# Performance work log

Hardware: AMD Instinct MI355X
Metric: run time of the kernel (lower is better)

Reference implementation:

```python
import jax, jax.numpy as jnp
import numpy as np


def conv1d(x, w, b):
    # x: [B, C_in, T], w: [C_out, C_in, K] (torch layout), b: [C_out]
    y = jax.lax.conv_general_dilated(
        x, w, window_strides=(1,), padding='SAME',
        dimension_numbers=('NCH', 'OIH', 'NCH'))
    return y + b[None, :, None]


def setup_inputs() -> dict:
    B, T, IN, H, D, K = 16, 2048, 80, 512, 512, 1024
    key = jax.random.key(0)
    ks = jax.random.split(key, 10)
    f32 = jnp.float32

    def w_init(k, shape, fan_in):
        return (jax.random.normal(k, shape, f32) / np.sqrt(fan_in)).astype(f32)

    return {
        'mels':    jax.random.normal(ks[0], (B, T, IN), f32),
        'enc_w1':  w_init(ks[1], (H, IN, 3), IN * 3),
        'enc_b1':  jnp.zeros((H,), f32),
        'enc_w2':  w_init(ks[2], (D, H, 3), H * 3),
        'enc_b2':  jnp.zeros((D,), f32),
        'codebook': jax.random.normal(ks[3], (K, D), f32),
        'dec_w1':  w_init(ks[4], (H, D, 3), D * 3),
        'dec_b1':  jnp.zeros((H,), f32),
        'dec_w2':  w_init(ks[5], (IN, H, 3), H * 3),
        'dec_b2':  jnp.zeros((IN,), f32),
    }


def reference(mels, enc_w1, enc_b1, enc_w2, enc_b2, codebook,
              dec_w1, dec_b1, dec_w2, dec_b2):
    B, T, _ = mels.shape
    D = codebook.shape[1]

    # ---- encoder: conv -> relu -> conv ----
    x = jnp.swapaxes(mels, 1, 2)                      # [B, in_dim, T]
    z = conv1d(jax.nn.relu(conv1d(x, enc_w1, enc_b1)), enc_w2, enc_b2)  # [B, D, T]

    # ---- vector quantization ----
    z_t = jnp.swapaxes(z, 1, 2)                       # [B, T, D]
    flat = z_t.reshape(-1, D)                         # [B*T, D]
    d = ((flat ** 2).sum(axis=1, keepdims=True)
         - 2.0 * flat @ codebook.T
         + (codebook ** 2).sum(axis=1)[None, :])      # [B*T, K]
    idx = jnp.argmin(d, axis=1).reshape(B, T)         # [B, T] int
    quantized = codebook[idx]                         # [B, T, D] gather

    # ---- decoder: conv -> relu -> conv ----
    q = jnp.swapaxes(quantized, 1, 2)                 # [B, D, T]
    recon = conv1d(jax.nn.relu(conv1d(q, dec_w1, dec_b1)), dec_w2, dec_b2)
    recon = jnp.swapaxes(recon, 1, 2)                 # [B, T, in_dim]
    return recon, idx
```

## Files before the change

### kernel.cpp

```cpp
#include <hip/hip_runtime.h>
#include <hip/hip_bf16.h>

#define Bsz   16
#define Tn    2048
#define INC   80
#define Hc    512
#define Dc    512
#define NCODE 1024
#define BT    (Bsz * Tn)
#define RECON_N (Bsz * Tn * INC)
#define MARGIN 0.03f

typedef __attribute__((ext_vector_type(8))) short bf16x8;
typedef __attribute__((ext_vector_type(4))) float f32x4;
typedef __attribute__((ext_vector_type(4))) unsigned short u16x4;

static __device__ __forceinline__ unsigned short f2bf(float x) {
    unsigned u = __float_as_uint(x);
    u += 0x7FFF + ((u >> 16) & 1);
    return (unsigned short)(u >> 16);
}
static __device__ __forceinline__ float bf2f(unsigned short h) {
    return __uint_as_float((unsigned)h << 16);
}

typedef const __attribute__((address_space(1))) unsigned int* gas_p;
typedef __attribute__((address_space(3))) unsigned int* las_p;
static __device__ __forceinline__ void async16(const void* g, const void* l) {
    __builtin_amdgcn_global_load_lds(
        (gas_p)(unsigned long long)g,
        (las_p)(unsigned int)(unsigned long long)l,
        16, 0, 0);
}

__global__ __launch_bounds__(64)
void code_norms(const float* __restrict__ CB, float* __restrict__ CN) {
    int j = blockIdx.x;
    int lane = threadIdx.x;
    const float4* row = (const float4*)(CB + (size_t)j * Dc);
    float s = 0.f;
    #pragma unroll
    for (int i = 0; i < 2; ++i) {
        float4 v = row[lane + i * 64];
        s = fmaf(v.x, v.x, s);
        s = fmaf(v.y, v.y, s);
        s = fmaf(v.z, v.z, s);
        s = fmaf(v.w, v.w, s);
    }
    #pragma unroll
    for (int off = 32; off > 0; off >>= 1) s += __shfl_down(s, off, 64);
    if (lane == 0) CN[j] = s;
}

__global__ __launch_bounds__(256)
void cb_transpose(const float* __restrict__ CB, float* __restrict__ CBt) {
    const int j0 = blockIdx.x * 64;
    const int d0 = blockIdx.y * 64;
    __shared__ float ts[64][65];
    const int tid = threadIdx.x;
    for (int i = tid; i < 4096; i += 256) {
        int r = i >> 6, c = i & 63;
        ts[r][c] = CB[(size_t)(j0 + r) * Dc + d0 + c];
    }
    __syncthreads();
    for (int i = tid; i < 4096; i += 256) {
        int r = i >> 6, c = i & 63;
        CBt[(size_t)(d0 + r) * NCODE + j0 + c] = ts[c][r];
    }
}

__global__ __launch_bounds__(256)
void mels_transpose(const float* __restrict__ M, float* __restrict__ MT) {
    const int t0 = blockIdx.x * 64;
    const int b  = blockIdx.y;
    __shared__ float ts[64][84];
    const int tid = threadIdx.x;
    #pragma unroll
    for (int it = 0; it < 5; ++it) {
        int i = tid + it * 256;
        int t = i / 20, c4 = i % 20;
        *(float4*)&ts[t][c4 * 4] =
            *(const float4*)&M[((size_t)b * Tn + t0 + t) * INC + c4 * 4];
    }
    __syncthreads();
    #pragma unroll
    for (int it = 0; it < 20; ++it) {
        int i = tid + it * 256;
        int c = i >> 6, t = i & 63;
        MT[((size_t)b * INC + c) * Tn + t0 + t] = ts[t][c];
    }
}

__global__ __launch_bounds__(256)
void wt_transpose(const float* __restrict__ W, float* __restrict__ Wt,
                  int Cin, int Cout) {
    const int o0 = blockIdx.x * 64;
    const int c0 = blockIdx.y * 16;
    __shared__ float ts[48][65];
    const int tid = threadIdx.x;
    for (int i = tid; i < 64 * 48; i += 256) {
        int o = i / 48, ck = i % 48;
        int oo = o0 + o;
        float v = 0.f;
        if (oo < Cout) v = W[(size_t)oo * Cin * 3 + c0 * 3 + ck];
        ts[ck][o] = v;
    }
    __syncthreads();
    for (int i = tid; i < 48 * 64; i += 256) {
        int o = i & 63, ck = i >> 6;
        int oo = o0 + o;
        if (oo < Cout) Wt[(size_t)(c0 * 3 + ck) * Cout + oo] = ts[ck][o];
    }
}

__global__ __launch_bounds__(256)
void wsplit(const float* __restrict__ W, unsigned short* __restrict__ Whi,
            unsigned short* __restrict__ Wlo) {
    int o = blockIdx.x, k = blockIdx.y;
    #pragma unroll
    for (int it = 0; it < 2; ++it) {
        int c = threadIdx.x + it * 256;
        float v = W[((size_t)o * Hc + c) * 3 + k];
        unsigned short h = f2bf(v);
        Whi[((size_t)k * Hc + o) * Hc + c] = h;
        Wlo[((size_t)k * Hc + o) * Hc + c] = f2bf(v - bf2f(h));
    }
}

__global__ __launch_bounds__(256)
void wsplit80(const float* __restrict__ W, unsigned short* __restrict__ Wh) {
    int o = blockIdx.x, k = blockIdx.y;
    #pragma unroll
    for (int it = 0; it < 2; ++it) {
        int c = threadIdx.x + it * 256;
        Wh[((size_t)k * INC + o) * Hc + c] = f2bf(W[((size_t)o * Hc + c) * 3 + k]);
    }
}

__global__ __launch_bounds__(256)
void cbsplit(const float* __restrict__ CB, unsigned short* __restrict__ CBh,
             unsigned short* __restrict__ CBl) {
    int j = blockIdx.x;
    #pragma unroll
    for (int it = 0; it < 2; ++it) {
        int d = threadIdx.x + it * 256;
        float v = CB[(size_t)j * Dc + d];
        unsigned short h = f2bf(v);
        CBh[(size_t)j * Dc + d] = h;
        CBl[(size_t)j * Dc + d] = f2bf(v - bf2f(h));
    }
}

__global__ __launch_bounds__(256)
void conv_enc1(const float* __restrict__ X, const float* __restrict__ Wt,
               const float* __restrict__ bias, float* __restrict__ Y) {
    const int t0 = blockIdx.x * 64;
    const int o0 = blockIdx.y * 128;
    const int b  = blockIdx.z;
    __shared__ __align__(16) float Xs[16][72];
    __shared__ __align__(16) float Ws[48][132];
    const int tid = threadIdx.x;
    const int tx = tid & 15, ty = tid >> 4;
    float acc[8][4] = {};
    const float* Xb = X + (size_t)b * INC * Tn;

    for (int c0 = 0; c0 < INC; c0 += 16) {
        for (int i = tid; i < 16 * 66; i += 256) {
            int cc = i / 66, tt = i % 66;
            int t = t0 + tt - 1;
            float v = 0.f;
            if (t >= 0 && t < Tn) v = Xb[(size_t)(c0 + cc) * Tn + t];
            Xs[cc][tt] = v;
        }
        for (int i = tid; i < 48 * 128; i += 256) {
            int o = i & 127, ck = i >> 7;
            Ws[ck][o] = Wt[(size_t)(c0 * 3 + ck) * Hc + o0 + o];
        }
        __syncthreads();
        #pragma unroll
        for (int cc = 0; cc < 16; ++cc) {
            float4 xa = *(const float4*)&Xs[cc][tx * 4];
            float2 xb2 = *(const float2*)&Xs[cc][tx * 4 + 4];
            float xv[6] = {xa.x, xa.y, xa.z, xa.w, xb2.x, xb2.y};
            #pragma unroll
            for (int k = 0; k < 3; ++k) {
                float4 wa = *(const float4*)&Ws[cc * 3 + k][ty * 4];
                float4 wb = *(const float4*)&Ws[cc * 3 + k][64 + ty * 4];
                float wv[8] = {wa.x, wa.y, wa.z, wa.w, wb.x, wb.y, wb.z, wb.w};
                #pragma unroll
                for (int i8 = 0; i8 < 8; ++i8)
                    #pragma unroll
                    for (int j = 0; j < 4; ++j)
                        acc[i8][j] = fmaf(wv[i8], xv[k + j], acc[i8][j]);
            }
        }
        __syncthreads();
    }
    float* Yb = Y + (size_t)b * Hc * Tn;
    #pragma unroll
    for (int og = 0; og < 2; ++og)
        #pragma unroll
        for (int oi = 0; oi < 4; ++oi) {
            int o = o0 + og * 64 + ty * 4 + oi;
            float bv = bias[o];
            const int i8 = og * 4 + oi;
            float4 r;
            r.x = fmaxf(acc[i8][0] + bv, 0.f);
            r.y = fmaxf(acc[i8][1] + bv, 0.f);
            r.z = fmaxf(acc[i8][2] + bv, 0.f);
            r.w = fmaxf(acc[i8][3] + bv, 0.f);
            *(float4*)&Yb[(size_t)o * Tn + t0 + tx * 4] = r;
        }
}

__global__ __launch_bounds__(256)
void zero_guards(unsigned short* __restrict__ Yhl) {
    const int b = blockIdx.x;
    u16x4 z = {0, 0, 0, 0};
    size_t r0 = (size_t)(b * (Tn + 2)) * 1024;
    size_t r1 = (size_t)(b * (Tn + 2) + Tn + 1) * 1024;
    *(u16x4*)(Yhl + r0 + threadIdx.x * 4) = z;
    *(u16x4*)(Yhl + r1 + threadIdx.x * 4) = z;
}

__global__ __launch_bounds__(256)
void split_t(const float* __restrict__ X, unsigned short* __restrict__ Yhl,
             int rowStride, int rowOff) {
    const int t0 = blockIdx.x * 64;
    const int c0 = blockIdx.y * 64;
    const int b  = blockIdx.z;
    __shared__ __align__(16) float ts[64][68];
    const int tid = threadIdx.x;
    #pragma unroll
    for (int it = 0; it < 4; ++it) {
        int i = tid + it * 256;
        int cc = i >> 4, t4 = i & 15;
        float4 v = *(const float4*)&X[((size_t)b * Hc + c0 + cc) * Tn + t0 + t4 * 4];
        ts[t4 * 4 + 0][cc] = v.x;
        ts[t4 * 4 + 1][cc] = v.y;
        ts[t4 * 4 + 2][cc] = v.z;
        ts[t4 * 4 + 3][cc] = v.w;
    }
    __syncthreads();
    #pragma unroll
    for (int it = 0; it < 4; ++it) {
        int i = tid + it * 256;
        int t = i >> 4, c4 = i & 15;
        int c = c0 + c4 * 4;
        float4 v = *(const float4*)&ts[t][c4 * 4];
        float va[4] = {v.x, v.y, v.z, v.w};
        u16x4 h, l;
        #pragma unroll
        for (int r = 0; r < 4; ++r) {
            unsigned short hh = f2bf(va[r]);
            h[r] = hh;
            l[r] = f2bf(va[r] - bf2f(hh));
        }
        size_t base = ((size_t)(b * rowStride + rowOff + t0 + t) * 16 + (c >> 5)) * 64
                      + (c & 31);
        *(u16x4*)(Yhl + base) = h;
        *(u16x4*)(Yhl + base + 32) = l;
    }
}

__global__ __launch_bounds__(256)
void conv_mid_mfma(const unsigned short* __restrict__ Xhl,
                   const unsigned short* __restrict__ Whi,
                   const unsigned short* __restrict__ Wlo,
                   const float* __restrict__ bias,
                   float* __restrict__ Y) {
    const int t0 = blockIdx.x * 128;
    const int o0 = blockIdx.y * 128;
    const int b  = blockIdx.z;
    __shared__ __align__(16) unsigned short XL[2][136 * 64];
    const int tid  = threadIdx.x;
    const int lane = tid & 63;
    const int wave = tid >> 6;
    const int wm = wave >> 1, wn = wave & 1;
    const int m16 = lane & 15;
    const int q = lane >> 4;
    const int lrow = lane >> 3;
    const int lchk = (lane & 7) ^ lrow;
    const unsigned short* Xb = Xhl + ((size_t)b * (Tn + 2) + t0) * 1024
                               + (size_t)lrow * 1024 + lchk * 8;

    f32x4 acc[4][4];
    #pragma unroll
    for (int mt = 0; mt < 4; ++mt)
        #pragma unroll
        for (int nt = 0; nt < 4; ++nt)
            acc[mt][nt] = (f32x4){0.f, 0.f, 0.f, 0.f};

    #pragma unroll
    for (int i = 0; i < 5; ++i) {
        int ii = wave + i * 4;
        if (ii < 17)
            async16(Xb + (size_t)ii * 8192, &XL[0][ii * 512]);
    }

    for (int c0 = 0; c0 < Hc; c0 += 32) {
        const int buf = (c0 >> 5) & 1;
        __syncthreads();
        if (c0 + 32 < Hc) {
            const unsigned short* src = Xb + (size_t)((c0 >> 5) + 1) * 64;
            #pragma unroll
            for (int i = 0; i < 5; ++i) {
                int ii = wave + i * 4;
                if (ii < 17)
                    async16(src + (size_t)ii * 8192, &XL[buf ^ 1][ii * 512]);
            }
        }
        #pragma unroll
        for (int k = 0; k < 3; ++k) {
            bf16x8 Ah[4], Al[4];
            #pragma unroll
            for (int mt = 0; mt < 4; ++mt) {
                int o = o0 + wm * 64 + mt * 16 + m16;
                size_t base = (size_t)(k * Hc + o) * Hc + c0 + q * 8;
                Ah[mt] = *(const bf16x8*)(Whi + base);
                Al[mt] = *(const bf16x8*)(Wlo + base);
            }
            #pragma unroll
            for (int nt = 0; nt < 4; ++nt) {
                int row = wn * 64 + nt * 16 + m16 + k;
                const unsigned short* rp = &XL[buf][row * 64];
                int ph = (q ^ (row & 7)) * 8;
                union { bf16x8 v; uint4 u; } bh, bl;
                bh.u = *(const uint4*)(rp + ph);
                bl.u = *(const uint4*)(rp + (ph ^ 32));
                #pragma unroll
                for (int mt = 0; mt < 4; ++mt)
                    acc[mt][nt] = __builtin_amdgcn_mfma_f32_16x16x32_bf16(
                        Ah[mt], bh.v, acc[mt][nt], 0, 0, 0);
                #pragma unroll
                for (int mt = 0; mt < 4; ++mt)
                    acc[mt][nt] = __builtin_amdgcn_mfma_f32_16x16x32_bf16(
                        Al[mt], bh.v, acc[mt][nt], 0, 0, 0);
                #pragma unroll
                for (int mt = 0; mt < 4; ++mt)
                    acc[mt][nt] = __builtin_amdgcn_mfma_f32_16x16x32_bf16(
                        Ah[mt], bl.v, acc[mt][nt], 0, 0, 0);
            }
        }
    }
    float* Yb = Y + (size_t)b * Hc * Tn;
    #pragma unroll
    for (int mt = 0; mt < 4; ++mt) {
        int ob = o0 + wm * 64 + mt * 16 + q * 4;
        float4 bq = *(const float4*)&bias[ob];
        float bqa[4] = {bq.x, bq.y, bq.z, bq.w};
        #pragma unroll
        for (int nt = 0; nt < 4; ++nt) {
            int t = t0 + wn * 64 + nt * 16 + m16;
            #pragma unroll
            for (int r = 0; r < 4; ++r)
                Yb[(size_t)(ob + r) * Tn + t] = acc[mt][nt][r] + bqa[r];
        }
    }
}

__global__ __launch_bounds__(256)
void dec2_mfma(const float* __restrict__ X,
               const unsigned short* __restrict__ Wh2,
               const float* __restrict__ bias, float* __restrict__ OUT) {
    const int t0 = blockIdx.x * 128;
    const int b  = blockIdx.z;
    __shared__ unsigned short Xs[2][130 * 36];
    const int tid = threadIdx.x;
    const int lane = tid & 63;
    const int wn = tid >> 6;
    const int m16 = lane & 15;
    const int q = lane >> 4;
    const float* Xb = X + (size_t)b * Hc * Tn;

    f32x4 acc[5][2];
    #pragma unroll
    for (int mt = 0; mt < 5; ++mt)
        #pragma unroll
        for (int nt = 0; nt < 2; ++nt)
            acc[mt][nt] = (f32x4){0.f, 0.f, 0.f, 0.f};

    float xr[17];
    #pragma unroll
    for (int it = 0; it < 17; ++it) {
        int f = tid + it * 256;
        if (it < 16 || tid < 64) {
            int cc = f / 130, tt = f - cc * 130;
            int t = t0 + tt - 1;
            xr[it] = (t >= 0 && t < Tn) ? Xb[(size_t)cc * Tn + t] : 0.f;
        }
    }

    for (int c0 = 0; c0 < Hc; c0 += 32) {
        const int buf = (c0 >> 5) & 1;
        #pragma unroll
        for (int it = 0; it < 17; ++it) {
            int f = tid + it * 256;
            if (it < 16 || tid < 64) {
                int cc = f / 130, tt = f - cc * 130;
                Xs[buf][tt * 36 + cc] = f2bf(xr[it]);
            }
        }
        __syncthreads();
        if (c0 + 32 < Hc) {
            const float* Xc = Xb + (size_t)(c0 + 32) * Tn;
            #pragma unroll
            for (int it = 0; it < 17; ++it) {
                int f = tid + it * 256;
                if (it < 16 || tid < 64) {
                    int cc = f / 130, tt = f - cc * 130;
                    int t = t0 + tt - 1;
                    xr[it] = (t >= 0 && t < Tn) ? Xc[(size_t)cc * Tn + t] : 0.f;
                }
            }
        }
        #pragma unroll
        for (int k = 0; k < 3; ++k) {
            bf16x8 Ah[5];
            #pragma unroll
            for (int mt = 0; mt < 5; ++mt) {
                int o = mt * 16 + m16;
                Ah[mt] = *(const bf16x8*)(Wh2 + ((size_t)(k * INC + o)) * Hc + c0 + q * 8);
            }
            #pragma unroll
            for (int nt = 0; nt < 2; ++nt) {
                int tt = wn * 32 + nt * 16 + m16 + k;
                union { bf16x8 v; uint2 h[2]; } bh;
                const unsigned short* ph = Xs[buf] + tt * 36 + q * 8;
                bh.h[0] = *(const uint2*)ph; bh.h[1] = *(const uint2*)(ph + 4);
                #pragma unroll
                for (int mt = 0; mt < 5; ++mt)
                    acc[mt][nt] = __builtin_amdgcn_mfma_f32_16x16x32_bf16(
                        Ah[mt], bh.v, acc[mt][nt], 0, 0, 0);
            }
        }
    }
    #pragma unroll
    for (int mt = 0; mt < 5; ++mt) {
        float4 bq = *(const float4*)&bias[mt * 16 + q * 4];
        #pragma unroll
        for (int nt = 0; nt < 2; ++nt) {
            int t = t0 + wn * 32 + nt * 16 + m16;
            float4 r;
            r.x = acc[mt][nt][0] + bq.x;
            r.y = acc[mt][nt][1] + bq.y;
            r.z = acc[mt][nt][2] + bq.z;
            r.w = acc[mt][nt][3] + bq.w;
            *(float4*)(OUT + ((size_t)b * Tn + t) * INC + mt * 16 + q * 4) = r;
        }
    }
}

__global__ __launch_bounds__(256)
void vq_mfma(const unsigned short* __restrict__ Zt,
             const unsigned short* __restrict__ CBh,
             const unsigned short* __restrict__ CBl,
             const float* __restrict__ CN,
             float* __restrict__ candv, int* __restrict__ candi,
             float* __restrict__ cand2v) {
    const int nb = blockIdx.x;
    const int jb = blockIdx.y;
    const int b  = nb >> 4;
    const int t0 = (nb & 15) * 128;
    const int jbase = jb * 128;
    __shared__ __align__(16) unsigned char pool[32768];
    unsigned short* XL0 = (unsigned short*)pool;
    unsigned short* XL1 = (unsigned short*)(pool + 16384);
    float* RV = (float*)pool;
    int*   RI = (int*)(pool + 4096);
    float* R2 = (float*)(pool + 8192);

    const int tid = threadIdx.x;
    const int lane = tid & 63;
    const int wave = tid >> 6;
    const int wm = wave >> 1, wn = wave & 1;
    const int m16 = lane & 15;
    const int q = lane >> 4;
    const int lrow = lane >> 3;
    const int lchk = (lane & 7) ^ lrow;
    const unsigned short* Zb = Zt + (size_t)(b * Tn + t0) * 1024
                               + (size_t)lrow * 1024 + lchk * 8;

    f32x4 acc[4][4];
    #pragma unroll
    for (int mt = 0; mt < 4; ++mt)
        #pragma unroll
        for (int nt = 0; nt < 4; ++nt)
            acc[mt][nt] = (f32x4){0.f, 0.f, 0.f, 0.f};

    #pragma unroll
    for (int i = 0; i < 4; ++i) {
        int ii = wave + i * 4;
        async16(Zb + (size_t)ii * 8192, XL0 + ii * 512);
    }

    for (int d0 = 0; d0 < Dc; d0 += 32) {
        const int buf = (d0 >> 5) & 1;
        unsigned short* XL = buf ? XL1 : XL0;
        __syncthreads();
        if (d0 + 32 < Dc) {
            unsigned short* XN = buf ? XL0 : XL1;
            const unsigned short* src = Zb + (size_t)((d0 >> 5) + 1) * 64;
            #pragma unroll
            for (int i = 0; i < 4; ++i) {
                int ii = wave + i * 4;
                async16(src + (size_t)ii * 8192, XN + ii * 512);
            }
        }
        bf16x8 Ah[4], Al[4];
        #pragma unroll
        for (int mt = 0; mt < 4; ++mt) {
            int j = jbase + wm * 64 + mt * 16 + m16;
            size_t base = (size_t)j * Dc + d0 + q * 8;
            Ah[mt] = *(const bf16x8*)(CBh + base);
            Al[mt] = *(const bf16x8*)(CBl + base);
        }
        #pragma unroll
        for (int nt = 0; nt < 4; ++nt) {
            int row = wn * 64 + nt * 16 + m16;
            const unsigned short* rp = XL + row * 64;
            int ph = (q ^ (row & 7)) * 8;
            union { bf16x8 v; uint4 u; } bh, bl;
            bh.u = *(const uint4*)(rp + ph);
            bl.u = *(const uint4*)(rp + (ph ^ 32));
            #pragma unroll
            for (int mt = 0; mt < 4; ++mt)
                acc[mt][nt] = __builtin_amdgcn_mfma_f32_16x16x32_bf16(
                    Ah[mt], bh.v, acc[mt][nt], 0, 0, 0);
            #pragma unroll
            for (int mt = 0; mt < 4; ++mt)
                acc[mt][nt] = __builtin_amdgcn_mfma_f32_16x16x32_bf16(
                    Al[mt], bh.v, acc[mt][nt], 0, 0, 0);
            #pragma unroll
            for (int mt = 0; mt < 4; ++mt)
                acc[mt][nt] = __builtin_amdgcn_mfma_f32_16x16x32_bf16(
                    Ah[mt], bl.v, acc[mt][nt], 0, 0, 0);
        }
    }
    __syncthreads();

    float cn4[4][4];
    #pragma unroll
    for (int mt = 0; mt < 4; ++mt) {
        float4 c = *(const float4*)&CN[jbase + wm * 64 + mt * 16 + q * 4];
        cn4[mt][0] = c.x; cn4[mt][1] = c.y; cn4[mt][2] = c.z; cn4[mt][3] = c.w;
    }
    #pragma unroll
    for (int nt = 0; nt < 4; ++nt) {
        int t = wn * 64 + nt * 16 + m16;
        float v1 = 1e30f, v2 = 1e30f;
        int i1 = 0;
        #pragma unroll
        for (int mt = 0; mt < 4; ++mt)
            #pragma unroll
            for (int r = 0; r < 4; ++r) {
                float d = fmaf(-2.f, acc[mt][nt][r], cn4[mt][r]);
                int j = jbase + wm * 64 + mt * 16 + q * 4 + r;
                if (d < v1 || (d == v1 && j < i1)) { v2 = v1; v1 = d; i1 = j; }
                else if (d < v2) v2 = d;
            }
        int slot = wm * 4 + q;
        RV[t * 8 + slot] = v1;
        RI[t * 8 + slot] = i1;
        R2[t * 8 + slot] = v2;
    }
    __syncthreads();
    if (tid < 128) {
        int t = tid;
        float v1 = RV[t * 8], v2 = R2[t * 8];
        int i1 = RI[t * 8];
        #pragma unroll
        for (int s = 1; s < 8; ++s) {
            float a1 = RV[t * 8 + s], a2 = R2[t * 8 + s];
            int ai = RI[t * 8 + s];
            if (a1 < v1 || (a1 == v1 && ai < i1)) {
                v2 = fminf(v1, a2); v1 = a1; i1 = ai;
            } else {
                v2 = fminf(v2, a1);
            }
        }
        int n = b * Tn + t0 + t;
        candv[(size_t)jb * BT + n] = v1;
        candi[(size_t)jb * BT + n] = i1;
        cand2v[(size_t)jb * BT + n] = v2;
    }
}

__global__ __launch_bounds__(256)
void vq_reduce2(const float* __restrict__ candv, const int* __restrict__ candi,
                const float* __restrict__ cand2v, int* __restrict__ idxI,
                float* __restrict__ idxf, int* __restrict__ flagn,
                int* __restrict__ flaglist) {
    int n = blockIdx.x * 256 + threadIdx.x;
    float v1 = candv[n], v2 = cand2v[n];
    int i1 = candi[n];
    #pragma unroll
    for (int jq = 1; jq < 8; ++jq) {
        float a1 = candv[(size_t)jq * BT + n];
        float a2 = cand2v[(size_t)jq * BT + n];
        int ai = candi[(size_t)jq * BT + n];
        if (a1 < v1 || (a1 == v1 && ai < i1)) {
            v2 = fminf(v1, a2); v1 = a1; i1 = ai;
        } else {
            v2 = fminf(v2, a1);
        }
    }
    idxI[n] = i1;
    idxf[n] = (float)i1;
    if (v2 - v1 < MARGIN) {
        int s = atomicAdd(flagn, 1);
        flaglist[s] = n;
    }
}

__global__ __launch_bounds__(256)
void vq_rescue(const int* __restrict__ flagn, const int* __restrict__ flaglist,
               const float* __restrict__ Z, const float* __restrict__ CB,
               const float* __restrict__ CN, int* __restrict__ idxI,
               float* __restrict__ idxf) {
    __shared__ float zs[512];
    __shared__ float rvv[256];
    __shared__ int   rii[256];
    const int nf = *flagn;
    for (int f = blockIdx.x; f < nf; f += gridDim.x) {
        int n = flaglist[f];
        int b = n / Tn, t = n - b * Tn;
        __syncthreads();
        #pragma unroll
        for (int it = 0; it < 2; ++it) {
            int d = threadIdx.x + it * 256;
            zs[d] = Z[((size_t)b * Dc + d) * Tn + t];
        }
        __syncthreads();
        float bv = 1e30f;
        int bi = 0;
        #pragma unroll
        for (int jj = 0; jj < 4; ++jj) {
            int j = threadIdx.x * 4 + jj;
            const float* cr = CB + (size_t)j * Dc;
            float dot = 0.f;
            for (int d = 0; d < Dc; ++d) dot = fmaf(zs[d], cr[d], dot);
            float dist = fmaf(-2.f, dot, CN[j]);
            if (dist < bv || (dist == bv && j < bi)) { bv = dist; bi = j; }
        }
        rvv[threadIdx.x] = bv;
        rii[threadIdx.x] = bi;
        __syncthreads();
        for (int off = 128; off > 0; off >>= 1) {
            if (threadIdx.x < off) {
                float ov = rvv[threadIdx.x + off];
                int oi = rii[threadIdx.x + off];
                if (ov < rvv[threadIdx.x] ||
                    (ov == rvv[threadIdx.x] && oi < rii[threadIdx.x])) {
                    rvv[threadIdx.x] = ov; rii[threadIdx.x] = oi;
                }
            }
            __syncthreads();
        }
        if (threadIdx.x == 0) {
            idxI[n] = rii[0];
            idxf[n] = (float)rii[0];
        }
    }
}

__global__ __launch_bounds__(256)
void gemm_g(const float* __restrict__ CBt, const float* __restrict__ Wt,
            float* __restrict__ G) {
    const int j0 = blockIdx.x * 64;
    const int kk = blockIdx.y >> 2;
    const int o0 = (blockIdx.y & 3) * 128;
    __shared__ __align__(16) float As[16][68];
    __shared__ __align__(16) float Bs[16][132];
    const int tid = threadIdx.x;
    const int tx = tid & 15, ty = tid >> 4;
    float acc[4][8] = {};

    for (int c0 = 0; c0 < Dc; c0 += 16) {
        {
            int cc = tid >> 4, j4 = tid & 15;
            *(float4*)&As[cc][j4 * 4] =
                *(const float4*)&CBt[(size_t)(c0 + cc) * NCODE + j0 + j4 * 4];
        }
        #pragma unroll
        for (int it = 0; it < 2; ++it) {
            int i = tid + it * 256;
            int cc = i >> 5, o4 = i & 31;
            *(float4*)&Bs[cc][o4 * 4] =
                *(const float4*)&Wt[(size_t)((c0 + cc) * 3 + kk) * Hc + o0 + o4 * 4];
        }
        __syncthreads();
        #pragma unroll
        for (int cc = 0; cc < 16; ++cc) {
            float4 a = *(const float4*)&As[cc][tx * 4];
            float av[4] = {a.x, a.y, a.z, a.w};
            float4 b0 = *(const float4*)&Bs[cc][ty * 4];
            float4 b1 = *(const float4*)&Bs[cc][64 + ty * 4];
            float bv[8] = {b0.x, b0.y, b0.z, b0.w, b1.x, b1.y, b1.z, b1.w};
            #pragma unroll
            for (int jj = 0; jj < 4; ++jj)
                #pragma unroll
                for (int oo = 0; oo < 8; ++oo)
                    acc[jj][oo] = fmaf(av[jj], bv[oo], acc[jj][oo]);
        }
        __syncthreads();
    }
    #pragma unroll
    for (int jj = 0; jj < 4; ++jj) {
        int j = j0 + tx * 4 + jj;
        float* gp = G + (size_t)j * 1536 + kk * 512 + o0;
        *(float4*)(gp + ty * 4) = *(float4*)&acc[jj][0];
        *(float4*)(gp + 64 + ty * 4) = *(float4*)&acc[jj][4];
    }
}

__global__ __launch_bounds__(256)
void dec_y3(const int* __restrict__ idx, const float* __restrict__ G,
            const float* __restrict__ bias, float* __restrict__ Y) {
    const int t0 = blockIdx.x * 64;
    const int o0 = blockIdx.y * 128;
    const int b  = blockIdx.z;
    const int tid = threadIdx.x;
    __shared__ int sidx[66];
    __shared__ __align__(16) float Ys[128][68];

    if (tid < 66) {
        int t = t0 + tid - 1;
        sidx[tid] = (t >= 0 && t < Tn) ? idx[b * Tn + t] : -1;
    }
    __syncthreads();

    const int o = tid & 127;
    const int half = tid >> 7;
    float acc[32] = {};
    #pragma unroll
    for (int kk = 0; kk < 3; ++kk) {
        const float* Gk = G + (size_t)kk * 512 + o0 + o;
        #pragma unroll
        for (int k = 0; k < 32; ++k) {
            int j = sidx[half + 2 * k + kk];
            if (j >= 0) acc[k] += Gk[(size_t)j * 1536];
        }
    }
    float bv = bias[o0 + o];
    #pragma unroll
    for (int k = 0; k < 32; ++k)
        Ys[o][half + 2 * k] = fmaxf(acc[k] + bv, 0.f);
    __syncthreads();

    float* Yb = Y + (size_t)b * Hc * Tn + t0;
    #pragma unroll
    for (int it = 0; it < 8; ++it) {
        int i = tid + it * 256;
        int t4 = i & 15, oo = i >> 4;
        *(float4*)&Yb[(size_t)(o0 + oo) * Tn + t4 * 4] =
            *(const float4*)&Ys[oo][t4 * 4];
    }
}

extern "C" void kernel_launch(void* const* d_in, const int* in_sizes, int n_in,
                              void* d_out, int out_size, void* d_ws, size_t ws_size,
                              hipStream_t stream) {
    const float* mels    = (const float*)d_in[0];
    const float* enc_w1  = (const float*)d_in[1];
    const float* enc_b1  = (const float*)d_in[2];
    const float* enc_w2  = (const float*)d_in[3];
    const float* enc_b2  = (const float*)d_in[4];
    const float* codebook= (const float*)d_in[5];
    const float* dec_w1  = (const float*)d_in[6];
    const float* dec_b1  = (const float*)d_in[7];
    const float* dec_w2  = (const float*)d_in[8];
    const float* dec_b2  = (const float*)d_in[9];

    float* out = (float*)d_out;
    float* recon = out;
    float* idxf  = out + RECON_N;

    const size_t ACT = (size_t)Bsz * Hc * Tn;
    const size_t Y1HL_U = (size_t)Bsz * (Tn + 2) * 1024 + 16384;
    const size_t R2F = Y1HL_U / 2;

    float* y1 = (float*)d_ws;
    float* zf = (float*)d_ws;
    float* y3 = (float*)d_ws;
    float* r2 = (float*)d_ws + ACT;
    float* melsT = r2;
    unsigned short* y1hl = (unsigned short*)r2;
    unsigned short* Zt   = (unsigned short*)r2;
    float* sm    = r2 + R2F;
    int*   idxI  = (int*)sm;
    float* cn    = (float*)(idxI + BT);
    float* cbt   = cn + NCODE;
    float* wt1   = cbt + (size_t)Dc * NCODE;
    float* wt3   = wt1 + (size_t)INC * 3 * Hc;
    float* candv = wt3 + (size_t)Dc * 3 * Hc;
    float* cand2v= candv + (size_t)8 * BT;
    int*   candi = (int*)(cand2v + (size_t)8 * BT);
    int*   flagn = candi + (size_t)8 * BT;
    int*   flaglist = flagn + 4;
    float* G     = (float*)(flaglist + BT);
    unsigned short* whi = (unsigned short*)(G + (size_t)NCODE * 1536);
    unsigned short* wlo = whi + (size_t)3 * Hc * Hc;
    unsigned short* cbh = wlo + (size_t)3 * Hc * Hc;
    unsigned short* cbl = cbh + (size_t)NCODE * Dc;
    unsigned short* wh2 = cbl + (size_t)NCODE * Dc;

    dim3 blk(256);
    hipMemsetAsync(flagn, 0, 16, stream);
    code_norms<<<dim3(NCODE), dim3(64), 0, stream>>>(codebook, cn);
    cb_transpose<<<dim3(NCODE / 64, Dc / 64), blk, 0, stream>>>(codebook, cbt);
    mels_transpose<<<dim3(Tn / 64, Bsz), blk, 0, stream>>>(mels, melsT);
    wt_transpose<<<dim3(Hc / 64, INC / 16), blk, 0, stream>>>(enc_w1, wt1, INC, Hc);
    wsplit<<<dim3(Hc, 3), blk, 0, stream>>>(enc_w2, whi, wlo);
    cbsplit<<<dim3(NCODE), blk, 0, stream>>>(codebook, cbh, cbl);
    wt_transpose<<<dim3(Hc / 64, Dc / 16), blk, 0, stream>>>(dec_w1, wt3, Dc, Hc);
    wsplit80<<<dim3(INC, 3), blk, 0, stream>>>(dec_w2, wh2);
    gemm_g<<<dim3(NCODE / 64, 12), blk, 0, stream>>>(cbt, wt3, G);
    conv_enc1<<<dim3(Tn / 64, Hc / 128, Bsz), blk, 0, stream>>>(melsT, wt1, enc_b1, y1);
    zero_guards<<<dim3(Bsz), blk, 0, stream>>>(y1hl);
    split_t<<<dim3(Tn / 64, Hc / 64, Bsz), blk, 0, stream>>>(y1, y1hl, Tn + 2, 1);
    conv_mid_mfma<<<dim3(Tn / 128, Hc / 128, Bsz), blk, 0, stream>>>(y1hl, whi, wlo,
                                                                     enc_b2, zf);
    split_t<<<dim3(Tn / 64, Hc / 64, Bsz), blk, 0, stream>>>(zf, Zt, Tn, 0);
    vq_mfma<<<dim3(BT / 128, NCODE / 128), blk, 0, stream>>>(Zt, cbh, cbl, cn,
                                                             candv, candi, cand2v);
    vq_reduce2<<<dim3(BT / 256), blk, 0, stream>>>(candv, candi, cand2v, idxI,
                                                   idxf, flagn, flaglist);
    vq_rescue<<<dim3(128), blk, 0, stream>>>(flagn, flaglist, zf, codebook, cn,
                                             idxI, idxf);
    dec_y3<<<dim3(Tn / 64, 4, Bsz), blk, 0, stream>>>(idxI, G, dec_b1, y3);
    dec2_mfma<<<dim3(Tn / 128, 1, Bsz), blk, 0, stream>>>(y3, wh2, dec_b2, recon);
}
```

Before: 831.4 us.

## Fuse bf16 hi/lo split into conv_enc1 epilogue and interleave split weight layouts

The first encoder conv now transposes its ReLU output through shared memory and writes the interleaved bf16 hi/lo time-major buffer directly. This removes the separate split_t pass and the fp32 intermediate round trip through global memory. The encoder weights and codebook hi/lo copies are packed into one interleaved array so each MFMA operand pair comes from neighbouring addresses. s_setprio is also raised around the MFMA bursts, and melsT is moved to its own workspace region because the aliasing plan changed.

After: 803.2 us. -3.4%, faster.

```diff
diff --git a/kernel.cpp b/kernel.cpp
--- a/kernel.cpp
+++ b/kernel.cpp
@@ -114,16 +114,16 @@
 }
 
 __global__ __launch_bounds__(256)
-void wsplit(const float* __restrict__ W, unsigned short* __restrict__ Whi,
-            unsigned short* __restrict__ Wlo) {
+void wsplit(const float* __restrict__ W, unsigned short* __restrict__ Whl) {
     int o = blockIdx.x, k = blockIdx.y;
     #pragma unroll
     for (int it = 0; it < 2; ++it) {
         int c = threadIdx.x + it * 256;
         float v = W[((size_t)o * Hc + c) * 3 + k];
         unsigned short h = f2bf(v);
-        Whi[((size_t)k * Hc + o) * Hc + c] = h;
-        Wlo[((size_t)k * Hc + o) * Hc + c] = f2bf(v - bf2f(h));
+        size_t base = ((size_t)(k * Hc + o) * 16 + (c >> 5)) * 64 + (c & 31);
+        Whl[base] = h;
+        Whl[base + 32] = f2bf(v - bf2f(h));
     }
 }
 
@@ -138,27 +138,32 @@
 }
 
 __global__ __launch_bounds__(256)
-void cbsplit(const float* __restrict__ CB, unsigned short* __restrict__ CBh,
-             unsigned short* __restrict__ CBl) {
+void cbsplit(const float* __restrict__ CB, unsigned short* __restrict__ CBhl) {
     int j = blockIdx.x;
     #pragma unroll
     for (int it = 0; it < 2; ++it) {
         int d = threadIdx.x + it * 256;
         float v = CB[(size_t)j * Dc + d];
         unsigned short h = f2bf(v);
-        CBh[(size_t)j * Dc + d] = h;
-        CBl[(size_t)j * Dc + d] = f2bf(v - bf2f(h));
+        size_t base = ((size_t)j * 16 + (d >> 5)) * 64 + (d & 31);
+        CBhl[base] = h;
+        CBhl[base + 32] = f2bf(v - bf2f(h));
     }
 }
 
 __global__ __launch_bounds__(256)
 void conv_enc1(const float* __restrict__ X, const float* __restrict__ Wt,
-               const float* __restrict__ bias, float* __restrict__ Y) {
+               const float* __restrict__ bias, unsigned short* __restrict__ Yhl) {
     const int t0 = blockIdx.x * 64;
     const int o0 = blockIdx.y * 128;
     const int b  = blockIdx.z;
-    __shared__ __align__(16) float Xs[16][72];
-    __shared__ __align__(16) float Ws[48][132];
+    union SharedU {
+        struct { float Xs[16][72]; float Ws[48][132]; } a;
+        float Ys[128][69];
+    };
+    __shared__ __align__(16) SharedU su;
+    float (&Xs)[16][72]  = su.a.Xs;
+    float (&Ws)[48][132] = su.a.Ws;
     const int tid = threadIdx.x;
     const int tx = tid & 15, ty = tid >> 4;
     float acc[8][4] = {};
@@ -196,21 +201,36 @@
         }
         __syncthreads();
     }
-    float* Yb = Y + (size_t)b * Hc * Tn;
     #pragma unroll
     for (int og = 0; og < 2; ++og)
         #pragma unroll
         for (int oi = 0; oi < 4; ++oi) {
-            int o = o0 + og * 64 + ty * 4 + oi;
-            float bv = bias[o];
+            int ol = og * 64 + ty * 4 + oi;
+            float bv = bias[o0 + ol];
             const int i8 = og * 4 + oi;
-            float4 r;
-            r.x = fmaxf(acc[i8][0] + bv, 0.f);
-            r.y = fmaxf(acc[i8][1] + bv, 0.f);
-            r.z = fmaxf(acc[i8][2] + bv, 0.f);
-            r.w = fmaxf(acc[i8][3] + bv, 0.f);
-            *(float4*)&Yb[(size_t)o * Tn + t0 + tx * 4] = r;
-        }
+            #pragma unroll
+            for (int j = 0; j < 4; ++j)
+                su.Ys[ol][tx * 4 + j] = fmaxf(acc[i8][j] + bv, 0.f);
+        }
+    __syncthreads();
+    #pragma unroll
+    for (int it = 0; it < 8; ++it) {
+        int i = tid + it * 256;
+        int oq = i & 31, t = i >> 5;
+        int o4 = o0 + oq * 4;
+        u16x4 h, l;
+        #pragma unroll
+        for (int r = 0; r < 4; ++r) {
+            float v = su.Ys[oq * 4 + r][t];
+            unsigned short hh = f2bf(v);
+            h[r] = hh;
+            l[r] = f2bf(v - bf2f(hh));
+        }
+        size_t base = ((size_t)(b * (Tn + 2) + 1 + t0 + t) * 16 + (o4 >> 5)) * 64
+                      + (o4 & 31);
+        *(u16x4*)(Yhl + base) = h;
+        *(u16x4*)(Yhl + base + 32) = l;
+    }
 }
 
 __global__ __launch_bounds__(256)
@@ -265,8 +285,7 @@
 
 __global__ __launch_bounds__(256)
 void conv_mid_mfma(const unsigned short* __restrict__ Xhl,
-                   const unsigned short* __restrict__ Whi,
-                   const unsigned short* __restrict__ Wlo,
+                   const unsigned short* __restrict__ Whl,
                    const float* __restrict__ bias,
                    float* __restrict__ Y) {
     const int t0 = blockIdx.x * 128;
@@ -316,9 +335,9 @@
             #pragma unroll
             for (int mt = 0; mt < 4; ++mt) {
                 int o = o0 + wm * 64 + mt * 16 + m16;
-                size_t base = (size_t)(k * Hc + o) * Hc + c0 + q * 8;
-                Ah[mt] = *(const bf16x8*)(Whi + base);
-                Al[mt] = *(const bf16x8*)(Wlo + base);
+                size_t base = ((size_t)(k * Hc + o) * 16 + (c0 >> 5)) * 64 + q * 8;
+                Ah[mt] = *(const bf16x8*)(Whl + base);
+                Al[mt] = *(const bf16x8*)(Whl + base + 32);
             }
             #pragma unroll
             for (int nt = 0; nt < 4; ++nt) {
@@ -328,6 +347,7 @@
                 union { bf16x8 v; uint4 u; } bh, bl;
                 bh.u = *(const uint4*)(rp + ph);
                 bl.u = *(const uint4*)(rp + (ph ^ 32));
+                __builtin_amdgcn_s_setprio(1);
                 #pragma unroll
                 for (int mt = 0; mt < 4; ++mt)
                     acc[mt][nt] = __builtin_amdgcn_mfma_f32_16x16x32_bf16(
@@ -340,6 +360,7 @@
                 for (int mt = 0; mt < 4; ++mt)
                     acc[mt][nt] = __builtin_amdgcn_mfma_f32_16x16x32_bf16(
                         Ah[mt], bl.v, acc[mt][nt], 0, 0, 0);
+                __builtin_amdgcn_s_setprio(0);
             }
         }
     }
@@ -453,8 +474,7 @@
 
 __global__ __launch_bounds__(256)
 void vq_mfma(const unsigned short* __restrict__ Zt,
-             const unsigned short* __restrict__ CBh,
-             const unsigned short* __restrict__ CBl,
+             const unsigned short* __restrict__ CBhl,
              const float* __restrict__ CN,
              float* __restrict__ candv, int* __restrict__ candi,
              float* __restrict__ cand2v) {
@@ -511,9 +531,9 @@
         #pragma unroll
         for (int mt = 0; mt < 4; ++mt) {
             int j = jbase + wm * 64 + mt * 16 + m16;
-            size_t base = (size_t)j * Dc + d0 + q * 8;
-            Ah[mt] = *(const bf16x8*)(CBh + base);
-            Al[mt] = *(const bf16x8*)(CBl + base);
+            size_t base = ((size_t)j * 16 + (d0 >> 5)) * 64 + q * 8;
+            Ah[mt] = *(const bf16x8*)(CBhl + base);
+            Al[mt] = *(const bf16x8*)(CBhl + base + 32);
         }
         #pragma unroll
         for (int nt = 0; nt < 4; ++nt) {
@@ -523,6 +543,7 @@
             union { bf16x8 v; uint4 u; } bh, bl;
             bh.u = *(const uint4*)(rp + ph);
             bl.u = *(const uint4*)(rp + (ph ^ 32));
+            __builtin_amdgcn_s_setprio(1);
             #pragma unroll
             for (int mt = 0; mt < 4; ++mt)
                 acc[mt][nt] = __builtin_amdgcn_mfma_f32_16x16x32_bf16(
@@ -535,6 +556,7 @@
             for (int mt = 0; mt < 4; ++mt)
                 acc[mt][nt] = __builtin_amdgcn_mfma_f32_16x16x32_bf16(
                     Ah[mt], bl.v, acc[mt][nt], 0, 0, 0);
+            __builtin_amdgcn_s_setprio(0);
         }
     }
     __syncthreads();
@@ -780,11 +802,9 @@
     const size_t Y1HL_U = (size_t)Bsz * (Tn + 2) * 1024 + 16384;
     const size_t R2F = Y1HL_U / 2;
 
-    float* y1 = (float*)d_ws;
     float* zf = (float*)d_ws;
     float* y3 = (float*)d_ws;
     float* r2 = (float*)d_ws + ACT;
-    float* melsT = r2;
     unsigned short* y1hl = (unsigned short*)r2;
     unsigned short* Zt   = (unsigned short*)r2;
     float* sm    = r2 + R2F;
@@ -799,11 +819,10 @@
     int*   flagn = candi + (size_t)8 * BT;
     int*   flaglist = flagn + 4;
     float* G     = (float*)(flaglist + BT);
-    unsigned short* whi = (unsigned short*)(G + (size_t)NCODE * 1536);
-    unsigned short* wlo = whi + (size_t)3 * Hc * Hc;
-    unsigned short* cbh = wlo + (size_t)3 * Hc * Hc;
-    unsigned short* cbl = cbh + (size_t)NCODE * Dc;
-    unsigned short* wh2 = cbl + (size_t)NCODE * Dc;
+    unsigned short* whl  = (unsigned short*)(G + (size_t)NCODE * 1536);
+    unsigned short* cbhl = whl + (size_t)3 * Hc * 1024;
+    unsigned short* wh2  = cbhl + (size_t)NCODE * 1024;
+    float* melsT = (float*)(wh2 + (size_t)3 * INC * Hc);
 
     dim3 blk(256);
     hipMemsetAsync(flagn, 0, 16, stream);
@@ -811,18 +830,18 @@
     cb_transpose<<<dim3(NCODE / 64, Dc / 64), blk, 0, stream>>>(codebook, cbt);
     mels_transpose<<<dim3(Tn / 64, Bsz), blk, 0, stream>>>(mels, melsT);
     wt_transpose<<<dim3(Hc / 64, INC / 16), blk, 0, stream>>>(enc_w1, wt1, INC, Hc);
-    wsplit<<<dim3(Hc, 3), blk, 0, stream>>>(enc_w2, whi, wlo);
-    cbsplit<<<dim3(NCODE), blk, 0, stream>>>(codebook, cbh, cbl);
+    wsplit<<<dim3(Hc, 3), blk, 0, stream>>>(enc_w2, whl);
+    cbsplit<<<dim3(NCODE), blk, 0, stream>>>(codebook, cbhl);
     wt_transpose<<<dim3(Hc / 64, Dc / 16), blk, 0, stream>>>(dec_w1, wt3, Dc, Hc);
     wsplit80<<<dim3(INC, 3), blk, 0, stream>>>(dec_w2, wh2);
     gemm_g<<<dim3(NCODE / 64, 12), blk, 0, stream>>>(cbt, wt3, G);
-    conv_enc1<<<dim3(Tn / 64, Hc / 128, Bsz), blk, 0, stream>>>(melsT, wt1, enc_b1, y1);
     zero_guards<<<dim3(Bsz), blk, 0, stream>>>(y1hl);
-    split_t<<<dim3(Tn / 64, Hc / 64, Bsz), blk, 0, stream>>>(y1, y1hl, Tn + 2, 1);
-    conv_mid_mfma<<<dim3(Tn / 128, Hc / 128, Bsz), blk, 0, stream>>>(y1hl, whi, wlo,
+    conv_enc1<<<dim3(Tn / 64, Hc / 128, Bsz), blk, 0, stream>>>(melsT, wt1, enc_b1,
+                                                                y1hl);
+    conv_mid_mfma<<<dim3(Tn / 128, Hc / 128, Bsz), blk, 0, stream>>>(y1hl, whl,
                                                                      enc_b2, zf);
     split_t<<<dim3(Tn / 64, Hc / 64, Bsz), blk, 0, stream>>>(zf, Zt, Tn, 0);
-    vq_mfma<<<dim3(BT / 128, NCODE / 128), blk, 0, stream>>>(Zt, cbh, cbl, cn,
+    vq_mfma<<<dim3(BT / 128, NCODE / 128), blk, 0, stream>>>(Zt, cbhl, cn,
                                                              candv, candi, cand2v);
     vq_reduce2<<<dim3(BT / 256), blk, 0, stream>>>(candv, candi, cand2v, idxI,
                                                    idxf, flagn, flaglist);
```
